# Kernel optimization log

Hardware: AMD Instinct MI355X
Metric: run time of the kernel (lower is better)

## Reference

```python
import jax, jax.numpy as jnp
import numpy as np

B, T, D, E = 4, 2048, 1024, 4096


def setup_inputs() -> dict:
    key = jax.random.key(0)
    ks = jax.random.split(key, 6)
    s = 0.02
    return {
        "x": jax.random.normal(ks[0], (B, T, D), jnp.float32),
        "W1": jax.random.normal(ks[1], (E, D), jnp.float32) * s,
        "b1": jnp.zeros((E,), jnp.float32),
        "W2": jax.random.normal(ks[2], (E, D), jnp.float32) * s,
        "b2": jnp.zeros((E,), jnp.float32),
        "Wg": jax.random.normal(ks[3], (2 * E, E), jnp.float32) * s,
        "bg": jnp.zeros((2 * E,), jnp.float32),
        "Wo": jax.random.normal(ks[4], (D, E), jnp.float32) * s,
        "bo": jnp.zeros((D,), jnp.float32),
    }


def _log_g(x):
    # log of g(x) where g(x) = x+0.5 for x>=0 else sigmoid(x)
    return jnp.where(x >= 0, jnp.log(jax.nn.relu(x) + 0.5), -jax.nn.softplus(-x))


def _min_gru(x_in, Wg, bg):
    # x_in: [B,T,E]; single linear -> (gate, candidate), log-space parallel scan, h0 = 0
    gh = jnp.einsum('bte,fe->btf', x_in, Wg) + bg
    gate, hidden = jnp.split(gh, 2, axis=-1)
    log_coeffs = -jax.nn.softplus(gate)          # log(1 - z)
    log_z = -jax.nn.softplus(-gate)              # log z
    log_values = log_z + _log_g(hidden)          # log(z * g(h_tilde))
    a_star = jnp.cumsum(log_coeffs, axis=1)      # Heinsen associative scan
    log_h = a_star + jax.lax.cumlogsumexp(log_values - a_star, axis=1)
    return jnp.exp(log_h)


def reference(x, W1, b1, W2, b2, Wg, bg, Wo, bo):
    x_in = jax.nn.silu(jnp.einsum('btd,ed->bte', x, W1) + b1)
    x_skip = jax.nn.silu(jnp.einsum('btd,ed->bte', x, W2) + b2)
    h = _min_gru(x_in, Wg, bg)
    return jnp.einsum('bte,de->btd', x_skip + h, Wo) + bo
```

## Files before the change

### kernel.cpp

```cpp
#include <hip/hip_runtime.h>
#include <cstdint>
#include <cstddef>

constexpr int CB  = 4;
constexpr int CT  = 2048;
constexpr int CD  = 1024;
constexpr int CE  = 4096;
constexpr int CM  = CB * CT;
constexpr int CN2E = 2 * CE;
constexpr int NCHUNK = 32;
constexpr int CLEN = CT / NCHUNK;

typedef float  f32x4  __attribute__((ext_vector_type(4)));
typedef __bf16 bf16x8 __attribute__((ext_vector_type(8)));

__device__ __forceinline__ unsigned short f2bf(float f) {
  unsigned int u = __float_as_uint(f);
  unsigned int r = u + 0x7FFFu + ((u >> 16) & 1u);
  return (unsigned short)(r >> 16);
}
__device__ __forceinline__ float bf2f(unsigned short h) {
  return __uint_as_float(((unsigned int)h) << 16);
}

__global__ __launch_bounds__(256) void k_f2bf4(const float* __restrict__ in,
                                               unsigned short* __restrict__ out, int n4) {
  int i = blockIdx.x * 256 + threadIdx.x;
  if (i >= n4) return;
  float4 v = ((const float4*)in)[i];
  ushort4 o;
  o.x = f2bf(v.x); o.y = f2bf(v.y); o.z = f2bf(v.z); o.w = f2bf(v.w);
  ((ushort4*)out)[i] = o;
}

__device__ __forceinline__ void gll16(const unsigned short* g, void* l) {
  __builtin_amdgcn_global_load_lds(
      (const __attribute__((address_space(1))) void*)g,
      (__attribute__((address_space(3))) void*)l, 16, 0, 0);
}

template <int EPI>
__global__ __launch_bounds__(512, 2) void gemm256(
    const unsigned short* __restrict__ A,
    const unsigned short* __restrict__ Bw,
    const float* __restrict__ bias0,
    const float* __restrict__ bias1,
    void* __restrict__ out0,
    void* __restrict__ out1,
    int M, int N, int K, int lda, int ld0, int esplit) {
  extern __shared__ char lds[];

  const int nbn = N >> 8;
  const int nbm = M >> 8;
  const int nwg = nbm * nbn;
  int bid = blockIdx.x;
  int tau = (bid & 7) * (nwg >> 3) + (bid >> 3);
  const int gsz = nbm * 4;
  int gg  = tau / gsz;
  int rem = tau - gg * gsz;
  const int bm = rem >> 2;
  const int bn = gg * 4 + (rem & 3);

  const int tid  = threadIdx.x;
  const int lane = tid & 63;
  const int wv   = tid >> 6;
  const int wr   = wv >> 2;
  const int wc   = wv & 3;

  const int sr2 = tid >> 2;
  const int scA = (((tid & 3) ^ ((sr2 >> 1) & 3)) * 8);

  const unsigned short* Abase = A  + (size_t)bm * 256 * lda;
  const unsigned short* Bbase = Bw + (size_t)bn * 256 * (size_t)K;
  const int NT = K >> 6;
  const int ldsw = wv * 1024;

  auto stage = [&](const unsigned short* Xb, int ldx, int xoff, int t, int ks) {
    char* base = lds + (t & 1) * 65536 + xoff + ks * 16384 + ldsw;
    const unsigned short* g = Xb + (size_t)t * 64 + ks * 32 + scA;
    gll16(g + (size_t)sr2 * ldx, base);
    gll16(g + (size_t)(sr2 + 128) * ldx, base + 8192);
  };

  const int lr = lane & 15, lk = lane >> 4;
  const int rch = (lk ^ ((lr >> 1) & 3)) * 16;
  const int aB = (wr * 128 + lr) * 64 + rch;
  const int bB = 32768 + (wc * 64 + lr) * 64 + rch;

  f32x4 acc[8][4];
#pragma unroll
  for (int m = 0; m < 8; m++)
#pragma unroll
    for (int n = 0; n < 4; n++) acc[m][n] = (f32x4){0.f, 0.f, 0.f, 0.f};

  stage(Abase, lda, 0, 0, 0); stage(Bbase, K, 32768, 0, 0);
  stage(Abase, lda, 0, 0, 1); stage(Bbase, K, 32768, 0, 1);

  for (int t = 0; t < NT; t++) {
    const char* bp = lds + (t & 1) * 65536;
    bf16x8 bfr[4], aq[4];
#pragma unroll
    for (int ph = 0; ph < 4; ph++) {
      const int ks = ph >> 1, mh = ph & 1;
      if (mh == 0) {
        if (t + 1 < NT || ks == 0) asm volatile("s_waitcnt vmcnt(4)" ::: "memory");
        else                       asm volatile("s_waitcnt vmcnt(0)" ::: "memory");
        __builtin_amdgcn_sched_barrier(0);
        __builtin_amdgcn_s_barrier();
        __builtin_amdgcn_sched_barrier(0);
      }
      const int ksb = ks * 16384;
#pragma unroll
      for (int i = 0; i < 4; i++)
        aq[i] = *(const bf16x8*)(bp + ksb + aB + (mh * 4 + i) * 1024);
      if (mh == 0) {
#pragma unroll
        for (int nf = 0; nf < 4; nf++)
          bfr[nf] = *(const bf16x8*)(bp + ksb + bB + nf * 1024);
      }
      if (t + 1 < NT) {
        if      (ph == 0) stage(Abase, lda, 0,     t + 1, 0);
        else if (ph == 1) stage(Bbase, K,   32768, t + 1, 0);
        else if (ph == 2) stage(Abase, lda, 0,     t + 1, 1);
        else              stage(Bbase, K,   32768, t + 1, 1);
      }
      __builtin_amdgcn_s_setprio(1);
#pragma unroll
      for (int i = 0; i < 4; i++)
#pragma unroll
        for (int nf = 0; nf < 4; nf++)
          acc[mh * 4 + i][nf] = __builtin_amdgcn_mfma_f32_16x16x32_bf16(
              aq[i], bfr[nf], acc[mh * 4 + i][nf], 0, 0, 0);
      __builtin_amdgcn_s_setprio(0);
    }
  }

  const int rb = bm * 256 + wr * 128 + (lane >> 4) * 4;
  const int cb = bn * 256 + wc * 64 + (lane & 15);
#pragma unroll
  for (int nf = 0; nf < 4; nf++) {
    const int col = cb + nf * 16;
    float bi;
    if (EPI == 0) bi = (col < esplit) ? bias0[col] : bias1[col - esplit];
    else          bi = bias0[col];
#pragma unroll
    for (int mf = 0; mf < 8; mf++) {
#pragma unroll
      for (int r = 0; r < 4; r++) {
        const int row = rb + mf * 16 + r;
        float v = acc[mf][nf][r] + bi;
        if (EPI == 0) {
          float sg = 1.f / (1.f + __expf(-v));
          unsigned short o = f2bf(v * sg);
          if (col < esplit) ((unsigned short*)out0)[(size_t)row * ld0 + col] = o;
          else              ((unsigned short*)out1)[(size_t)row * ld0 + (col - esplit)] = o;
        } else if (EPI == 1) {
          ((float*)out0)[(size_t)row * ld0 + col] = v;
        } else {
          unsigned short o;
          if (col < esplit) {
            float e = __expf(-fabsf(v));
            float inv = 1.f / (1.f + e);
            o = f2bf((v >= 0.f) ? e * inv : inv);
          } else {
            float gf;
            if (v >= 0.f) gf = v + 0.5f;
            else { float eh = __expf(v); gf = eh / (1.f + eh); }
            o = f2bf(gf);
          }
          ((unsigned short*)out0)[(size_t)row * ld0 + col] = o;
        }
      }
    }
  }
}

__global__ __launch_bounds__(256) void k_scan1(const unsigned short* __restrict__ ghc,
                                               float* __restrict__ Ac,
                                               float* __restrict__ Bc) {
  int tid = threadIdx.x;
  int lane = tid & 63, cw = tid >> 6;
  int bid = blockIdx.x;
  int eg = bid & 63;
  int cq = bid >> 6;
  int chunk = cq * 4 + cw;
  int e = eg * 64 + lane;
  const unsigned short* cp = ghc + (size_t)(chunk * CLEN) * CN2E + e;
  float h = 0.f, A = 1.f;
#pragma unroll 8
  for (int t = 0; t < CLEN; t++) {
    float c  = bf2f(cp[(size_t)t * CN2E]);
    float gf = bf2f(cp[(size_t)t * CN2E + CE]);
    float v  = (1.f - c) * gf;
    h = __builtin_fmaf(c, h, v);
    A *= c;
  }
  Ac[(size_t)chunk * CE + e] = A;
  Bc[(size_t)chunk * CE + e] = h;
}

__global__ __launch_bounds__(256) void k_scan2(const float* __restrict__ Ac,
                                               const float* __restrict__ Bc,
                                               float* __restrict__ Hs) {
  int e = blockIdx.x * 256 + threadIdx.x;
  float h = 0.f;
#pragma unroll
  for (int ch = 0; ch < NCHUNK; ch++) {
    Hs[(size_t)ch * CE + e] = h;
    h = __builtin_fmaf(Ac[(size_t)ch * CE + e], h, Bc[(size_t)ch * CE + e]);
  }
}

__global__ __launch_bounds__(256) void k_scan3(const unsigned short* __restrict__ ghc,
                                               const float* __restrict__ Hs,
                                               const unsigned short* __restrict__ xs,
                                               unsigned short* __restrict__ sp) {
  int tid = threadIdx.x;
  int lane = tid & 63, cw = tid >> 6;
  int bid = blockIdx.x;
  int eg = bid & 63;
  int cq = bid >> 6;
  int chunk = cq * 4 + cw;
  int e = eg * 64 + lane;
  float h = Hs[(size_t)chunk * CE + e];
  const unsigned short* cp  = ghc + (size_t)(chunk * CLEN) * CN2E + e;
  const unsigned short* xsp = xs  + (size_t)(chunk * CLEN) * CE + e;
  unsigned short*       spp = sp  + (size_t)(chunk * CLEN) * CE + e;
#pragma unroll 4
  for (int t = 0; t < CLEN; t++) {
    float c  = bf2f(cp[(size_t)t * CN2E]);
    float gf = bf2f(cp[(size_t)t * CN2E + CE]);
    float v  = (1.f - c) * gf;
    h = __builtin_fmaf(c, h, v);
    float s = h + bf2f(xsp[(size_t)t * CE]);
    spp[(size_t)t * CE] = f2bf(s);
  }
}

extern "C" void kernel_launch(void* const* d_in, const int* in_sizes, int n_in,
                              void* d_out, int out_size, void* d_ws, size_t ws_size,
                              hipStream_t stream) {
  const float* x  = (const float*)d_in[0];
  const float* W1 = (const float*)d_in[1];
  const float* b1 = (const float*)d_in[2];
  const float* W2 = (const float*)d_in[3];
  const float* b2 = (const float*)d_in[4];
  const float* Wg = (const float*)d_in[5];
  const float* bg = (const float*)d_in[6];
  const float* Wo = (const float*)d_in[7];
  const float* bo = (const float*)d_in[8];
  float* out = (float*)d_out;

  const size_t MB = 1024 * 1024;
  if (ws_size < 234 * MB) return;
  char* ws = (char*)d_ws;
  unsigned short* wgb   = (unsigned short*)(ws);
  unsigned short* wob   = (unsigned short*)(ws + 64 * MB);
  unsigned short* wcat  = (unsigned short*)(ws + 72 * MB);
  unsigned short* xb    = (unsigned short*)(ws + 88 * MB);
  unsigned short* ghc   = (unsigned short*)(ws + 72 * MB);
  unsigned short* xin   = (unsigned short*)(ws + 104 * MB);
  unsigned short* xskip = (unsigned short*)(ws + 168 * MB);
  float* Ac = (float*)(ws + 232 * MB);
  float* Bc = (float*)(ws + 232 * MB + 512 * 1024);
  float* Hs = (float*)(ws + 233 * MB);

  hipFuncSetAttribute(reinterpret_cast<const void*>(&gemm256<0>),
                      hipFuncAttributeMaxDynamicSharedMemorySize, 131072);
  hipFuncSetAttribute(reinterpret_cast<const void*>(&gemm256<1>),
                      hipFuncAttributeMaxDynamicSharedMemorySize, 131072);
  hipFuncSetAttribute(reinterpret_cast<const void*>(&gemm256<2>),
                      hipFuncAttributeMaxDynamicSharedMemorySize, 131072);

  {
    int n4;
    n4 = CM * CD / 4;   k_f2bf4<<<n4 / 256, 256, 0, stream>>>(x,  xb,   n4);
    n4 = CE * CD / 4;   k_f2bf4<<<n4 / 256, 256, 0, stream>>>(W1, wcat, n4);
    n4 = CE * CD / 4;   k_f2bf4<<<n4 / 256, 256, 0, stream>>>(W2, wcat + (size_t)CE * CD, n4);
    n4 = CN2E * CE / 4; k_f2bf4<<<n4 / 256, 256, 0, stream>>>(Wg, wgb,  n4);
    n4 = CD * CE / 4;   k_f2bf4<<<n4 / 256, 256, 0, stream>>>(Wo, wob,  n4);
  }

  gemm256<0><<<(CM / 256) * (CN2E / 256), 512, 131072, stream>>>(
      xb, wcat, b1, b2, xin, xskip, CM, CN2E, CD, CD, CE, CE);

  for (int b = 0; b < CB; b++) {
    const unsigned short* xin_b = xin + (size_t)b * CT * CE;
    gemm256<2><<<(CT / 256) * (CN2E / 256), 512, 131072, stream>>>(
        xin_b, wgb, bg, nullptr, ghc, nullptr, CT, CN2E, CE, CE, CN2E, CE);
    k_scan1<<<512, 256, 0, stream>>>(ghc, Ac, Bc);
    k_scan2<<<CE / 256, 256, 0, stream>>>(Ac, Bc, Hs);
    k_scan3<<<512, 256, 0, stream>>>(ghc, Hs, xskip + (size_t)b * CT * CE,
                                     xin + (size_t)b * CT * CE);
  }

  gemm256<1><<<(CM / 256) * (CD / 256), 512, 131072, stream>>>(
      xin, wob, bo, nullptr, out, nullptr, CM, CD, CE, CE, CD, 0);
}
```

Measured before the change: 940.8 us.

## Switch GEMM inner loop to 32x32x16 MFMA tiles with reworked barrier placement

Replaces the 16x16x32 bf16 MFMA fragments with 32x32x16 MFMA instructions, so each wave holds a 4x2 grid of 16-wide accumulators instead of 8x4 four-wide ones. LDS fragment addressing and the epilogue row/column mapping are rewritten to match. The vmcnt wait and barrier move from the start of each k-step to after the MFMAs, with extra barriers and lgkmcnt waits each phase. Larger MFMA tiles can cut LDS reads per FLOP and instruction issue, but the added barriers per phase may cost synchronization overhead.

```diff
diff --git a/kernel.cpp b/kernel.cpp
--- a/kernel.cpp
+++ b/kernel.cpp
@@ -11,8 +11,9 @@
 constexpr int NCHUNK = 32;
 constexpr int CLEN = CT / NCHUNK;
 
-typedef float  f32x4  __attribute__((ext_vector_type(4)));
-typedef __bf16 bf16x8 __attribute__((ext_vector_type(8)));
+typedef float  f32x4   __attribute__((ext_vector_type(4)));
+typedef float  f32x16  __attribute__((ext_vector_type(16)));
+typedef __bf16 bf16x8  __attribute__((ext_vector_type(8)));
 
 __device__ __forceinline__ unsigned short f2bf(float f) {
   unsigned int u = __float_as_uint(f);
@@ -82,41 +83,44 @@
     gll16(g + (size_t)(sr2 + 128) * ldx, base + 8192);
   };
 
-  const int lr = lane & 15, lk = lane >> 4;
-  const int rch = (lk ^ ((lr >> 1) & 3)) * 16;
-  const int aB = (wr * 128 + lr) * 64 + rch;
-  const int bB = 32768 + (wc * 64 + lr) * 64 + rch;
-
-  f32x4 acc[8][4];
-#pragma unroll
-  for (int m = 0; m < 8; m++)
-#pragma unroll
-    for (int n = 0; n < 4; n++) acc[m][n] = (f32x4){0.f, 0.f, 0.f, 0.f};
+  const int r32 = lane & 31;
+  const int kh  = lane >> 5;
+  const int swz = (r32 >> 1) & 3;
+  const int ck2[2] = { ((0 + kh) ^ swz) * 16, ((2 + kh) ^ swz) * 16 };
+  const int aRow0 = (wr * 128 + r32) * 64;
+  const int bRow0 = 32768 + (wc * 64 + r32) * 64;
+
+  f32x16 acc[4][2];
+#pragma unroll
+  for (int m = 0; m < 4; m++)
+#pragma unroll
+    for (int n = 0; n < 2; n++) acc[m][n] = (f32x16)(0.f);
 
   stage(Abase, lda, 0, 0, 0); stage(Bbase, K, 32768, 0, 0);
   stage(Abase, lda, 0, 0, 1); stage(Bbase, K, 32768, 0, 1);
+  asm volatile("s_waitcnt vmcnt(4)" ::: "memory");
+  __builtin_amdgcn_sched_barrier(0);
+  __builtin_amdgcn_s_barrier();
 
   for (int t = 0; t < NT; t++) {
     const char* bp = lds + (t & 1) * 65536;
-    bf16x8 bfr[4], aq[4];
+    bf16x8 bfr[2][2];
 #pragma unroll
     for (int ph = 0; ph < 4; ph++) {
       const int ks = ph >> 1, mh = ph & 1;
+      const int ksb = ks * 16384;
+      bf16x8 aq[2][2];
+#pragma unroll
+      for (int q = 0; q < 2; q++)
+#pragma unroll
+        for (int kl = 0; kl < 2; kl++)
+          aq[q][kl] = *(const bf16x8*)(bp + ksb + aRow0 + (mh * 2 + q) * 2048 + ck2[kl]);
       if (mh == 0) {
-        if (t + 1 < NT || ks == 0) asm volatile("s_waitcnt vmcnt(4)" ::: "memory");
-        else                       asm volatile("s_waitcnt vmcnt(0)" ::: "memory");
-        __builtin_amdgcn_sched_barrier(0);
-        __builtin_amdgcn_s_barrier();
-        __builtin_amdgcn_sched_barrier(0);
-      }
-      const int ksb = ks * 16384;
-#pragma unroll
-      for (int i = 0; i < 4; i++)
-        aq[i] = *(const bf16x8*)(bp + ksb + aB + (mh * 4 + i) * 1024);
-      if (mh == 0) {
-#pragma unroll
-        for (int nf = 0; nf < 4; nf++)
-          bfr[nf] = *(const bf16x8*)(bp + ksb + bB + nf * 1024);
+#pragma unroll
+        for (int nf = 0; nf < 2; nf++)
+#pragma unroll
+          for (int kl = 0; kl < 2; kl++)
+            bfr[nf][kl] = *(const bf16x8*)(bp + ksb + bRow0 + nf * 2048 + ck2[kl]);
       }
       if (t + 1 < NT) {
         if      (ph == 0) stage(Abase, lda, 0,     t + 1, 0);
@@ -124,30 +128,41 @@
         else if (ph == 2) stage(Abase, lda, 0,     t + 1, 1);
         else              stage(Bbase, K,   32768, t + 1, 1);
       }
+      __builtin_amdgcn_s_barrier();
+      asm volatile("s_waitcnt lgkmcnt(0)" ::: "memory");
+      __builtin_amdgcn_sched_barrier(0);
       __builtin_amdgcn_s_setprio(1);
 #pragma unroll
-      for (int i = 0; i < 4; i++)
-#pragma unroll
-        for (int nf = 0; nf < 4; nf++)
-          acc[mh * 4 + i][nf] = __builtin_amdgcn_mfma_f32_16x16x32_bf16(
-              aq[i], bfr[nf], acc[mh * 4 + i][nf], 0, 0, 0);
+      for (int kl = 0; kl < 2; kl++)
+#pragma unroll
+        for (int q = 0; q < 2; q++)
+#pragma unroll
+          for (int nf = 0; nf < 2; nf++)
+            acc[mh * 2 + q][nf] = __builtin_amdgcn_mfma_f32_32x32x16_bf16(
+                aq[q][kl], bfr[nf][kl], acc[mh * 2 + q][nf], 0, 0, 0);
       __builtin_amdgcn_s_setprio(0);
+      if (mh == 1) {
+        if (t + 1 < NT) asm volatile("s_waitcnt vmcnt(4)" ::: "memory");
+        else if (ks == 0) asm volatile("s_waitcnt vmcnt(0)" ::: "memory");
+        __builtin_amdgcn_sched_barrier(0);
+      }
+      __builtin_amdgcn_s_barrier();
     }
   }
 
-  const int rb = bm * 256 + wr * 128 + (lane >> 4) * 4;
-  const int cb = bn * 256 + wc * 64 + (lane & 15);
-#pragma unroll
-  for (int nf = 0; nf < 4; nf++) {
-    const int col = cb + nf * 16;
+  const int rb = bm * 256 + wr * 128 + (lane >> 5) * 4;
+  const int cb = bn * 256 + wc * 64 + (lane & 31);
+#pragma unroll
+  for (int nf = 0; nf < 2; nf++) {
+    const int col = cb + nf * 32;
     float bi;
     if (EPI == 0) bi = (col < esplit) ? bias0[col] : bias1[col - esplit];
     else          bi = bias0[col];
 #pragma unroll
-    for (int mf = 0; mf < 8; mf++) {
-#pragma unroll
-      for (int r = 0; r < 4; r++) {
-        const int row = rb + mf * 16 + r;
+    for (int mf = 0; mf < 4; mf++) {
+#pragma unroll
+      for (int r = 0; r < 16; r++) {
+        const int row = rb + mf * 32 + (r & 3) + 8 * (r >> 2);
         float v = acc[mf][nf][r] + bi;
         if (EPI == 0) {
           float sg = 1.f / (1.f + __expf(-v));
```

New measurement: 1.043 ms. +10.9%, slower.

## Make GEMM K a template parameter and restructure per-phase barrier/waitcnt schedule

Applied to the files above, without the earlier changes.

The GEMM's K dimension becomes a compile-time template parameter, so the tile-loop trip count is constant and the loop can be unrolled by two. The in-loop synchronisation is reorganised. The first wait now happens before the loop, and each phase has barriers plus an lgkmcnt(0) wait placed between the LDS fragment loads and the MFMAs. The global-load vmcnt waits move to the end of each k-half. The goal is a tighter, lockstep ping-pong schedule between waves, at the cost of more barriers per iteration and a risk of extra stalls or race-sensitive ordering.

```diff
diff --git a/kernel.cpp b/kernel.cpp
--- a/kernel.cpp
+++ b/kernel.cpp
@@ -11,8 +11,8 @@
 constexpr int NCHUNK = 32;
 constexpr int CLEN = CT / NCHUNK;
 
-typedef float  f32x4  __attribute__((ext_vector_type(4)));
-typedef __bf16 bf16x8 __attribute__((ext_vector_type(8)));
+typedef float  f32x4   __attribute__((ext_vector_type(4)));
+typedef __bf16 bf16x8  __attribute__((ext_vector_type(8)));
 
 __device__ __forceinline__ unsigned short f2bf(float f) {
   unsigned int u = __float_as_uint(f);
@@ -39,7 +39,7 @@
       (__attribute__((address_space(3))) void*)l, 16, 0, 0);
 }
 
-template <int EPI>
+template <int EPI, int K>
 __global__ __launch_bounds__(512, 2) void gemm256(
     const unsigned short* __restrict__ A,
     const unsigned short* __restrict__ Bw,
@@ -47,7 +47,7 @@
     const float* __restrict__ bias1,
     void* __restrict__ out0,
     void* __restrict__ out1,
-    int M, int N, int K, int lda, int ld0, int esplit) {
+    int M, int N, int lda, int ld0, int esplit) {
   extern __shared__ char lds[];
 
   const int nbn = N >> 8;
@@ -72,7 +72,7 @@
 
   const unsigned short* Abase = A  + (size_t)bm * 256 * lda;
   const unsigned short* Bbase = Bw + (size_t)bn * 256 * (size_t)K;
-  const int NT = K >> 6;
+  constexpr int NT = K >> 6;
   const int ldsw = wv * 1024;
 
   auto stage = [&](const unsigned short* Xb, int ldx, int xoff, int t, int ks) {
@@ -95,20 +95,17 @@
 
   stage(Abase, lda, 0, 0, 0); stage(Bbase, K, 32768, 0, 0);
   stage(Abase, lda, 0, 0, 1); stage(Bbase, K, 32768, 0, 1);
-
+  asm volatile("s_waitcnt vmcnt(4)" ::: "memory");
+  __builtin_amdgcn_sched_barrier(0);
+  __builtin_amdgcn_s_barrier();
+
+#pragma unroll 2
   for (int t = 0; t < NT; t++) {
     const char* bp = lds + (t & 1) * 65536;
     bf16x8 bfr[4], aq[4];
 #pragma unroll
     for (int ph = 0; ph < 4; ph++) {
       const int ks = ph >> 1, mh = ph & 1;
-      if (mh == 0) {
-        if (t + 1 < NT || ks == 0) asm volatile("s_waitcnt vmcnt(4)" ::: "memory");
-        else                       asm volatile("s_waitcnt vmcnt(0)" ::: "memory");
-        __builtin_amdgcn_sched_barrier(0);
-        __builtin_amdgcn_s_barrier();
-        __builtin_amdgcn_sched_barrier(0);
-      }
       const int ksb = ks * 16384;
 #pragma unroll
       for (int i = 0; i < 4; i++)
@@ -124,6 +121,9 @@
         else if (ph == 2) stage(Abase, lda, 0,     t + 1, 1);
         else              stage(Bbase, K,   32768, t + 1, 1);
       }
+      __builtin_amdgcn_s_barrier();
+      asm volatile("s_waitcnt lgkmcnt(0)" ::: "memory");
+      __builtin_amdgcn_sched_barrier(0);
       __builtin_amdgcn_s_setprio(1);
 #pragma unroll
       for (int i = 0; i < 4; i++)
@@ -132,6 +132,12 @@
           acc[mh * 4 + i][nf] = __builtin_amdgcn_mfma_f32_16x16x32_bf16(
               aq[i], bfr[nf], acc[mh * 4 + i][nf], 0, 0, 0);
       __builtin_amdgcn_s_setprio(0);
+      if (mh == 1) {
+        if (t + 1 < NT) asm volatile("s_waitcnt vmcnt(4)" ::: "memory");
+        else if (ks == 0) asm volatile("s_waitcnt vmcnt(0)" ::: "memory");
+        __builtin_amdgcn_sched_barrier(0);
+      }
+      __builtin_amdgcn_s_barrier();
     }
   }
 
@@ -265,11 +271,11 @@
   float* Bc = (float*)(ws + 232 * MB + 512 * 1024);
   float* Hs = (float*)(ws + 233 * MB);
 
-  hipFuncSetAttribute(reinterpret_cast<const void*>(&gemm256<0>),
+  hipFuncSetAttribute(reinterpret_cast<const void*>(&gemm256<0, CD>),
                       hipFuncAttributeMaxDynamicSharedMemorySize, 131072);
-  hipFuncSetAttribute(reinterpret_cast<const void*>(&gemm256<1>),
+  hipFuncSetAttribute(reinterpret_cast<const void*>(&gemm256<1, CE>),
                       hipFuncAttributeMaxDynamicSharedMemorySize, 131072);
-  hipFuncSetAttribute(reinterpret_cast<const void*>(&gemm256<2>),
+  hipFuncSetAttribute(reinterpret_cast<const void*>(&gemm256<2, CE>),
                       hipFuncAttributeMaxDynamicSharedMemorySize, 131072);
 
   {
@@ -281,19 +287,19 @@
     n4 = CD * CE / 4;   k_f2bf4<<<n4 / 256, 256, 0, stream>>>(Wo, wob,  n4);
   }
 
-  gemm256<0><<<(CM / 256) * (CN2E / 256), 512, 131072, stream>>>(
-      xb, wcat, b1, b2, xin, xskip, CM, CN2E, CD, CD, CE, CE);
+  gemm256<0, CD><<<(CM / 256) * (CN2E / 256), 512, 131072, stream>>>(
+      xb, wcat, b1, b2, xin, xskip, CM, CN2E, CD, CE, CE);
 
   for (int b = 0; b < CB; b++) {
     const unsigned short* xin_b = xin + (size_t)b * CT * CE;
-    gemm256<2><<<(CT / 256) * (CN2E / 256), 512, 131072, stream>>>(
-        xin_b, wgb, bg, nullptr, ghc, nullptr, CT, CN2E, CE, CE, CN2E, CE);
+    gemm256<2, CE><<<(CT / 256) * (CN2E / 256), 512, 131072, stream>>>(
+        xin_b, wgb, bg, nullptr, ghc, nullptr, CT, CN2E, CE, CN2E, CE);
     k_scan1<<<512, 256, 0, stream>>>(ghc, Ac, Bc);
     k_scan2<<<CE / 256, 256, 0, stream>>>(Ac, Bc, Hs);
     k_scan3<<<512, 256, 0, stream>>>(ghc, Hs, xskip + (size_t)b * CT * CE,
                                      xin + (size_t)b * CT * CE);
   }
 
-  gemm256<1><<<(CM / 256) * (CD / 256), 512, 131072, stream>>>(
-      xin, wob, bo, nullptr, out, nullptr, CM, CD, CE, CE, CD, 0);
-}
+  gemm256<1, CE><<<(CM / 256) * (CD / 256), 512, 131072, stream>>>(
+      xin, wob, bo, nullptr, out, nullptr, CM, CD, CE, CD, 0);
+}
```

Measured after the change: 959.8 us. +2.0%, slower.
